# Kernel optimization log

Hardware: AMD Instinct MI355X
Metric: run time of the kernel (lower is better)

## Reference

```python
import jax, jax.numpy as jnp
import numpy as np

EPS_LN = 1e-5
EPS_BN = 1e-5


def ln_channels(x, w, b):
    # LayerNorm2d: normalize over channel dim of NCHW
    mu = x.mean(axis=1, keepdims=True)
    var = x.var(axis=1, keepdims=True)
    return (x - mu) / jnp.sqrt(var + EPS_LN) * w[None, :, None, None] + b[None, :, None, None]


def bn_eval(x, g, b):
    # eval-mode BatchNorm2d with running_mean=0, running_var=1
    return x / jnp.sqrt(1.0 + EPS_BN) * g[None, :, None, None] + b[None, :, None, None]


def conv1x1(x, w, b):
    return jnp.einsum('bchw,oc->bohw', x, w) + b[None, :, None, None]


def q_shift(x):
    # directional shift: 4 channel quarters shifted right/left/down/up by 1 px (zero pad)
    C = x.shape[1]
    q = C // 4
    return jnp.concatenate([
        jnp.pad(x[:, 0 * q:1 * q, :, :-1], ((0, 0), (0, 0), (0, 0), (1, 0))),
        jnp.pad(x[:, 1 * q:2 * q, :, 1:], ((0, 0), (0, 0), (0, 0), (0, 1))),
        jnp.pad(x[:, 2 * q:3 * q, :-1, :], ((0, 0), (0, 0), (1, 0), (0, 0))),
        jnp.pad(x[:, 3 * q:4 * q, 1:, :], ((0, 0), (0, 0), (0, 1), (0, 0))),
    ], axis=1)


def wkv_scan(k, v, w_neg, u):
    # numerically-stable RWKV WKV recurrence. k, v: [N, T, C]; w_neg (negative decay), u: [C]
    N, T, C = k.shape

    def step(carry, kv):
        a, b, p = carry
        kt, vt = kv
        q = jnp.maximum(p, u + kt)
        e1 = jnp.exp(p - q)
        e2 = jnp.exp(u + kt - q)
        out = (e1 * a + e2 * vt) / (e1 * b + e2)
        q2 = jnp.maximum(p + w_neg, kt)
        f1 = jnp.exp(p + w_neg - q2)
        f2 = jnp.exp(kt - q2)
        return (f1 * a + f2 * vt, f1 * b + f2, q2), out

    init = (jnp.zeros((N, C), k.dtype), jnp.zeros((N, C), k.dtype), jnp.full((N, C), -1e38, k.dtype))
    _, outs = jax.lax.scan(step, init, (jnp.swapaxes(k, 0, 1), jnp.swapaxes(v, 0, 1)))
    return jnp.swapaxes(outs, 0, 1)


def shape_guided_rwkv(x, mask, mix_k, mix_v, mix_r, Wk, Wv, Wr, Wo, decay, first, kn_w, kn_b):
    B, C, H, W = x.shape
    xs = q_shift(x)
    x_sh = mask * xs + (1.0 - mask) * x  # saliency-guided shift blend
    mk = mix_k[None, :, None, None]
    mv = mix_v[None, :, None, None]
    mr = mix_r[None, :, None, None]
    xk = x * mk + x_sh * (1.0 - mk)
    xv = x * mv + x_sh * (1.0 - mv)
    xr = x * mr + x_sh * (1.0 - mr)
    k = jnp.einsum('bchw,oc->bohw', xk, Wk)
    v = jnp.einsum('bchw,oc->bohw', xv, Wv)
    sr = jax.nn.sigmoid(jnp.einsum('bchw,oc->bohw', xr, Wr))
    w_neg = -jnp.exp(decay)
    # horizontal orientation: scan each row left->right
    kh = k.transpose(0, 2, 3, 1).reshape(B * H, W, C)
    vh = v.transpose(0, 2, 3, 1).reshape(B * H, W, C)
    wkv_h = wkv_scan(kh, vh, w_neg, first).reshape(B, H, W, C).transpose(0, 3, 1, 2)
    # vertical orientation: scan each column top->bottom
    kv_ = k.transpose(0, 3, 2, 1).reshape(B * W, H, C)
    vv_ = v.transpose(0, 3, 2, 1).reshape(B * W, H, C)
    wkv_v = wkv_scan(kv_, vv_, w_neg, first).reshape(B, W, H, C).transpose(0, 3, 2, 1)
    wkv = 0.5 * (wkv_h + wkv_v)
    wkv = ln_channels(wkv, kn_w, kn_b)  # key_norm=True
    out = jnp.einsum('bchw,oc->bohw', sr * wkv, Wo)
    return x + out


def channel_fusion(x, c1_w, c1_b, bn1_g, bn1_b, c2_w, c2_b, bn2_g, bn2_b, c3_w, c3_b, bn3_g, bn3_b):
    # grouped 3x3 conv (groups=2) -> GELU -> BN -> 1x1 expand -> GELU -> BN -> 1x1 reduce -> GELU -> BN
    y = jax.lax.conv_general_dilated(x, c1_w, (1, 1), 'SAME',
                                     dimension_numbers=('NCHW', 'OIHW', 'NCHW'),
                                     feature_group_count=2) + c1_b[None, :, None, None]
    y = bn_eval(jax.nn.gelu(y, approximate=False), bn1_g, bn1_b)
    y = bn_eval(jax.nn.gelu(conv1x1(y, c2_w, c2_b), approximate=False), bn2_g, bn2_b)
    y = bn_eval(jax.nn.gelu(conv1x1(y, c3_w, c3_b), approximate=False), bn3_g, bn3_b)
    return y


def patch_expand(x, up_w, up_b, s=2):
    B, C, H, W = x.shape
    y = conv1x1(x, up_w, up_b)  # [B, Cout*s*s, H, W]
    Cout = y.shape[1] // (s * s)
    y = y.reshape(B, Cout, s, s, H, W).transpose(0, 1, 4, 2, 5, 3).reshape(B, Cout, H * s, W * s)
    return y


def setup_inputs() -> dict:
    key = jax.random.key(0)
    B, C, Cs, Cout, H, W, s = 8, 256, 512, 128, 64, 64, 2
    ks = jax.random.split(key, 32)
    sc = C ** -0.5
    inp = {
        'x': jax.random.normal(ks[0], (B, C, H, W), jnp.float32),
        'skip': jax.random.normal(ks[1], (B, Cs, H, W), jnp.float32),
        'saliency_mask': jax.random.uniform(ks[2], (B, 1, H, W), jnp.float32),
        'ln1_w': jnp.ones((C,)), 'ln1_b': jnp.zeros((C,)),
        'ln2_w': jnp.ones((C,)), 'ln2_b': jnp.zeros((C,)),
        'mix_k': jax.random.uniform(ks[3], (C,)),
        'mix_v': jax.random.uniform(ks[4], (C,)),
        'mix_r': jax.random.uniform(ks[5], (C,)),
        'Wk': jax.random.normal(ks[6], (C, C)) * sc,
        'Wv': jax.random.normal(ks[7], (C, C)) * sc,
        'Wr': jax.random.normal(ks[8], (C, C)) * sc,
        'Wo': jax.random.normal(ks[9], (C, C)) * sc,
        'decay': jax.random.normal(ks[10], (C,)) * 0.5,
        'first': jax.random.normal(ks[11], (C,)) * 0.5,
        'kn_w': jnp.ones((C,)), 'kn_b': jnp.zeros((C,)),
        'sp_w': jax.random.normal(ks[12], (C, Cs)) * (Cs ** -0.5),
        'sp_b': jnp.zeros((C,)),
        'c1_w': jax.random.normal(ks[13], (2 * C, C, 3, 3)) * ((C * 9) ** -0.5),
        'c1_b': jnp.zeros((2 * C,)),
        'bn1_g': jnp.ones((2 * C,)), 'bn1_b': jnp.zeros((2 * C,)),
        'c2_w': jax.random.normal(ks[14], (4 * C, 2 * C)) * ((2 * C) ** -0.5),
        'c2_b': jnp.zeros((4 * C,)),
        'bn2_g': jnp.ones((4 * C,)), 'bn2_b': jnp.zeros((4 * C,)),
        'c3_w': jax.random.normal(ks[15], (C, 4 * C)) * ((4 * C) ** -0.5),
        'c3_b': jnp.zeros((C,)),
        'bn3_g': jnp.ones((C,)), 'bn3_b': jnp.zeros((C,)),
        'up_w': jax.random.normal(ks[16], (Cout * s * s, C)) * sc,
        'up_b': jnp.zeros((Cout * s * s,)),
    }
    return inp


def reference(x, skip, saliency_mask, ln1_w, ln1_b, ln2_w, ln2_b, mix_k, mix_v, mix_r,
              Wk, Wv, Wr, Wo, decay, first, kn_w, kn_b, sp_w, sp_b,
              c1_w, c1_b, bn1_g, bn1_b, c2_w, c2_b, bn2_g, bn2_b, c3_w, c3_b, bn3_g, bn3_b,
              up_w, up_b):
    xn = ln_channels(x, ln1_w, ln1_b)
    x_sg = shape_guided_rwkv(xn, saliency_mask, mix_k, mix_v, mix_r, Wk, Wv, Wr, Wo,
                             decay, first, kn_w, kn_b)
    skip_feat = conv1x1(skip, sp_w, sp_b)
    x_cat = jnp.concatenate([x_sg, skip_feat], axis=1)
    x_fused = channel_fusion(x_cat, c1_w, c1_b, bn1_g, bn1_b, c2_w, c2_b, bn2_g, bn2_b,
                             c3_w, c3_b, bn3_g, bn3_b)
    x_fused = ln_channels(x_fused, ln2_w, ln2_b)
    return patch_expand(x_fused, up_w, up_b, s=2)
```

## Files before the change

### kernel.cpp

```cpp
#include <hip/hip_runtime.h>
#include <hip/hip_bf16.h>
#include <math.h>

#define B_ 8
#define C_ 256
#define P_ 4096

typedef __bf16 bf16_t;
typedef __attribute__((ext_vector_type(8))) __bf16 bf16x8;
typedef __attribute__((ext_vector_type(4))) __bf16 bf16x4;
typedef __attribute__((ext_vector_type(4))) float f32x4;

template<typename T, int TRANS, int TROUT>
__global__ __launch_bounds__(256)
void ln_stats_kernel(const T* __restrict__ in, float2* __restrict__ stats,
                     bf16_t* __restrict__ outT)
{
    __shared__ float sred[4][64];
    __shared__ float s2red[4][64];
    int tid = threadIdx.x;
    if (TRANS) {
        int wp = tid >> 2, cw = tid & 3;
        int gp = blockIdx.x * 64 + wp;
        const bf16_t* row = (const bf16_t*)in + (size_t)gp * 256 + cw * 64;
        float s = 0.f, s2 = 0.f;
        #pragma unroll
        for (int i = 0; i < 64; i += 8) {
            bf16x8 v = *reinterpret_cast<const bf16x8*>(&row[i]);
            #pragma unroll
            for (int j = 0; j < 8; ++j) {
                float f = (float)v[j]; s += f; s2 += f * f;
            }
        }
        sred[cw][wp] = s; s2red[cw][wp] = s2;
        __syncthreads();
        if (cw == 0) {
            s  = sred[0][wp]  + sred[1][wp]  + sred[2][wp]  + sred[3][wp];
            s2 = s2red[0][wp] + s2red[1][wp] + s2red[2][wp] + s2red[3][wp];
            float mu  = s * (1.f / 256.f);
            float var = s2 * (1.f / 256.f) - mu * mu;
            stats[gp] = make_float2(mu, 1.0f / sqrtf(var + 1e-5f));
        }
        return;
    }
    int wp = tid & 63, cw = tid >> 6;
    int gp = blockIdx.x * 64 + wp;
    int b  = gp >> 12, p = gp & 4095;
    size_t base = (size_t)b * 256 * 4096 + p;
    float s = 0.f, s2 = 0.f;
    bf16x8 chunk;
    #pragma unroll 8
    for (int cc = 0; cc < 64; ++cc) {
        float v = (float)in[base + (size_t)(cw * 64 + cc) * 4096];
        s += v; s2 += v * v;
        if (TROUT) {
            chunk[cc & 7] = (bf16_t)v;
            if ((cc & 7) == 7)
                *reinterpret_cast<bf16x8*>(
                    &outT[(size_t)gp * 256 + cw * 64 + (cc & ~7)]) = chunk;
        }
    }
    sred[cw][wp] = s; s2red[cw][wp] = s2;
    __syncthreads();
    if (cw == 0) {
        s  = sred[0][wp]  + sred[1][wp]  + sred[2][wp]  + sred[3][wp];
        s2 = s2red[0][wp] + s2red[1][wp] + s2red[2][wp] + s2red[3][wp];
        float mu  = s * (1.f / 256.f);
        float var = s2 * (1.f / 256.f) - mu * mu;
        stats[gp] = make_float2(mu, 1.0f / sqrtf(var + 1e-5f));
    }
}

__global__ __launch_bounds__(256)
void skip_transpose_kernel(const float* __restrict__ in, bf16_t* __restrict__ outT)
{
    __shared__ bf16_t t[64 * 66];
    int p0 = blockIdx.x << 6;
    int c0 = blockIdx.y << 6;
    int b  = blockIdx.z;
    int tid = threadIdx.x;
    int pl = tid & 63, cq = tid >> 6;
    const float* src = in + ((size_t)b * 512 + c0) * 4096 + p0;
    #pragma unroll
    for (int i = 0; i < 16; ++i) {
        int cl = i * 4 + cq;
        t[pl * 66 + cl] = (bf16_t)src[(size_t)cl * 4096 + pl];
    }
    __syncthreads();
    int pw = tid >> 2, ch = tid & 3;
    bf16x8 v0 = *reinterpret_cast<const bf16x8*>(&t[pw * 66 + ch * 16]);
    bf16x8 v1 = *reinterpret_cast<const bf16x8*>(&t[pw * 66 + ch * 16 + 8]);
    bf16_t* dst = outT + ((size_t)b * 4096 + p0 + pw) * 512 + c0 + ch * 16;
    *reinterpret_cast<bf16x8*>(dst) = v0;
    *reinterpret_cast<bf16x8*>(dst + 8) = v1;
}

__global__ __launch_bounds__(256)
void qshift_mix_kernel(const float* __restrict__ x, const float2* __restrict__ st1,
                       const float* __restrict__ mask,
                       const float* __restrict__ gw, const float* __restrict__ gb,
                       const float* __restrict__ mk_, const float* __restrict__ mv_,
                       const float* __restrict__ mr_,
                       bf16_t* __restrict__ xk, bf16_t* __restrict__ xv,
                       bf16_t* __restrict__ xr)
{
    int gid = blockIdx.x * 256 + threadIdx.x;
    int g = gid << 3;
    int p = g & 4095;
    int c = (g >> 12) & 255;
    int b = g >> 20;
    int h = p >> 6, w0 = p & 63;
    float gwc = gw[c], gbc = gb[c];
    int sbase = (b << 12) + p;

    float4 x0 = *reinterpret_cast<const float4*>(&x[g]);
    float4 x1 = *reinterpret_cast<const float4*>(&x[g + 4]);
    float xv8[8] = {x0.x, x0.y, x0.z, x0.w, x1.x, x1.y, x1.z, x1.w};
    float2 s8[8];
    #pragma unroll
    for (int i = 0; i < 4; ++i) {
        float4 t = *reinterpret_cast<const float4*>(&st1[sbase + i * 2]);
        s8[2 * i]     = make_float2(t.x, t.y);
        s8[2 * i + 1] = make_float2(t.z, t.w);
    }
    float xn8[8];
    #pragma unroll
    for (int i = 0; i < 8; ++i)
        xn8[i] = (xv8[i] - s8[i].x) * s8[i].y * gwc + gbc;

    float xs8[8];
    int quad = c >> 6;
    if (quad == 0) {
        xs8[0] = 0.f;
        if (w0 > 0) {
            float xm = x[g - 1]; float2 sm = st1[sbase - 1];
            xs8[0] = (xm - sm.x) * sm.y * gwc + gbc;
        }
        #pragma unroll
        for (int i = 1; i < 8; ++i) xs8[i] = xn8[i - 1];
    } else if (quad == 1) {
        #pragma unroll
        for (int i = 0; i < 7; ++i) xs8[i] = xn8[i + 1];
        xs8[7] = 0.f;
        if (w0 + 8 < 64) {
            float xp = x[g + 8]; float2 sp = st1[sbase + 8];
            xs8[7] = (xp - sp.x) * sp.y * gwc + gbc;
        }
    } else {
        int d = (quad == 2) ? -64 : 64;
        bool ok = (quad == 2) ? (h > 0) : (h < 63);
        if (ok) {
            float4 y0 = *reinterpret_cast<const float4*>(&x[g + d]);
            float4 y1 = *reinterpret_cast<const float4*>(&x[g + d + 4]);
            float yv8[8] = {y0.x, y0.y, y0.z, y0.w, y1.x, y1.y, y1.z, y1.w};
            #pragma unroll
            for (int i = 0; i < 4; ++i) {
                float4 t = *reinterpret_cast<const float4*>(&st1[sbase + d + i * 2]);
                float2 sa = make_float2(t.x, t.y), sb = make_float2(t.z, t.w);
                xs8[2 * i]     = (yv8[2 * i]     - sa.x) * sa.y * gwc + gbc;
                xs8[2 * i + 1] = (yv8[2 * i + 1] - sb.x) * sb.y * gwc + gbc;
            }
        } else {
            #pragma unroll
            for (int i = 0; i < 8; ++i) xs8[i] = 0.f;
        }
    }

    float4 m0 = *reinterpret_cast<const float4*>(&mask[sbase]);
    float4 m1 = *reinterpret_cast<const float4*>(&mask[sbase + 4]);
    float mm[8] = {m0.x, m0.y, m0.z, m0.w, m1.x, m1.y, m1.z, m1.w};
    float xsh8[8];
    #pragma unroll
    for (int i = 0; i < 8; ++i)
        xsh8[i] = mm[i] * xs8[i] + (1.f - mm[i]) * xn8[i];

    float ak = mk_[c], av = mv_[c], ar = mr_[c];
    bf16x8 ok_, ov_, or_;
    #pragma unroll
    for (int i = 0; i < 8; ++i) {
        ok_[i] = (bf16_t)(ak * xn8[i] + (1.f - ak) * xsh8[i]);
        ov_[i] = (bf16_t)(av * xn8[i] + (1.f - av) * xsh8[i]);
        or_[i] = (bf16_t)(ar * xn8[i] + (1.f - ar) * xsh8[i]);
    }
    *reinterpret_cast<bf16x8*>(&xk[g]) = ok_;
    *reinterpret_cast<bf16x8*>(&xv[g]) = ov_;
    *reinterpret_cast<bf16x8*>(&xr[g]) = or_;
}

#define EP_NONE    0
#define EP_SIGMOID 1
#define EP_BIAS    2
#define EP_RESLN   3
#define EP_GELU_BN 4
#define EP_SHUFFLE 5
#define EP_KVR     6
#define EP_WOSKIP  7

template<int NB, int BMODE, int EPI, int OUTBF, int TILE, int OTR>
__global__ __launch_bounds__(256, (TILE == 64) ? 4 : 2)
void mfma_gemm(const bf16_t* __restrict__ Wp, const void* __restrict__ Xin,
               const bf16_t* __restrict__ X2,
               const float2* __restrict__ bstats, const float* __restrict__ blnw,
               const float* __restrict__ blnb,
               const float* __restrict__ bias, const bf16_t* __restrict__ skipT,
               const float* __restrict__ bng, const float* __restrict__ bnb,
               const float* __restrict__ resx, const float2* __restrict__ estats,
               const float* __restrict__ elnw, const float* __restrict__ elnb,
               void* __restrict__ OutV,
               int O, int K, int Cstride, int obs, int ocoff)
{
    constexpr int MI = TILE / 32;
    constexpr int BROWS = (NB == 3) ? 2 * 66 : TILE;
    __shared__ bf16_t Alds[NB * TILE * 36];
    __shared__ bf16_t Blds[BROWS * 36];
    int tid = threadIdx.x;
    int bx = blockIdx.x;
    int o0 = blockIdx.y * TILE;
    int b  = blockIdx.z;
    int p0 = bx * TILE;
    int cbase = (NB == 3) ? ((o0 >> 8) << 8) : 0;

    bool wo = true;
    int bb = b;
    if (EPI == EP_WOSKIP) { wo = (b >> 3) != 0; bb = b & 7; }

    const bf16_t* Wpe = Wp;
    if (EPI == EP_KVR)    Wpe = Wp + (size_t)(b >> 3) * O * K;
    if (EPI == EP_WOSKIP) Wpe = wo ? Wp : (Wp + 65536);
    int Krun = K;
    if (EPI == EP_WOSKIP) Krun = wo ? 256 : 512;

    int lane = tid & 63, wid = tid >> 6;
    int l15 = lane & 15;
    int lk8 = (lane >> 4) << 3;
    int mbase = (wid >> 1) * (TILE / 2);
    int nbase = (wid & 1) * (TILE / 2);

    const bf16_t* Xb_bf = (const bf16_t*)Xin + (size_t)bb * Cstride * 4096;
    const float*  Xb_f  = (const float*)Xin + (size_t)bb * Cstride * 4096;
    const bf16_t* X2b   = (BMODE == 3) ? X2 + (size_t)bb * Cstride * 4096 : nullptr;
    const bf16_t* skb   = (EPI == EP_WOSKIP)
                          ? skipT + (size_t)bb * 4096 * 512 : nullptr;

    f32x4 acc[MI][MI] = {};

    if (NB == 3 && tid < 144) {
        int r = tid / 72, rest = tid % 72;
        int col = rest / 36, cc = rest % 36;
        Blds[(r * 66 + (col ? 65 : 0)) * 36 + cc] = (bf16_t)0.f;
    }

    for (int kh = 0; kh < NB; ++kh) {
        for (int c0 = 0; c0 < Krun; c0 += 32) {
            __syncthreads();
            if (NB == 3) {
                #pragma unroll
                for (int q = 0; q < 2; ++q) {
                    int cid = tid + q * 256;
                    int r   = cid >> 8;
                    int w   = (cid >> 2) & 63;
                    int ch4 = cid & 3;
                    int hr  = (bx << 1) + kh - 1 + r;
                    bf16x8 bv;
                    #pragma unroll
                    for (int i = 0; i < 8; ++i) bv[i] = (bf16_t)0.f;
                    if (hr >= 0 && hr < 64)
                        bv = *reinterpret_cast<const bf16x8*>(
                               Xb_bf + (size_t)((hr << 6) + w) * 512
                                     + cbase + c0 + ch4 * 8);
                    *reinterpret_cast<bf16x8*>(
                        &Blds[(r * 66 + w + 1) * 36 + ch4 * 8]) = bv;
                }
            } else if (BMODE >= 4) {
                constexpr int NCH = (TILE == 128) ? 2 : 1;
                #pragma unroll
                for (int q = 0; q < NCH; ++q) {
                    int cid = tid + q * 256;
                    int p   = cid >> 2;
                    int ch4 = cid & 3;
                    bf16x8 bv = *reinterpret_cast<const bf16x8*>(
                        Xb_bf + (size_t)(p0 + p) * Cstride + c0 + ch4 * 8);
                    if (BMODE == 5) {
                        float2 st = bstats[(bb << 12) + p0 + p];
                        #pragma unroll
                        for (int j = 0; j < 8; ++j) {
                            int cc = c0 + ch4 * 8 + j;
                            bv[j] = (bf16_t)(((float)bv[j] - st.x) * st.y
                                             * blnw[cc] + blnb[cc]);
                        }
                    }
                    *reinterpret_cast<bf16x8*>(&Blds[p * 36 + ch4 * 8]) = bv;
                }
            } else if (EPI == EP_WOSKIP) {
                int p = tid >> 2, ch4 = tid & 3;
                if (!wo) {
                    bf16x8 bv = *reinterpret_cast<const bf16x8*>(
                        skb + (size_t)(p0 + p) * 512 + c0 + ch4 * 8);
                    *reinterpret_cast<bf16x8*>(&Blds[p * 36 + ch4 * 8]) = bv;
                } else {
                    bf16x8 wv = *reinterpret_cast<const bf16x8*>(
                        Xb_bf + (size_t)(p0 + p) * 256 + c0 + ch4 * 8);
                    bf16x8 rv = *reinterpret_cast<const bf16x8*>(
                        X2b + (size_t)(p0 + p) * 256 + c0 + ch4 * 8);
                    float2 st = bstats[(bb << 12) + p0 + p];
                    bf16x8 bv;
                    #pragma unroll
                    for (int j = 0; j < 8; ++j) {
                        int cc = c0 + ch4 * 8 + j;
                        float v = ((float)wv[j] - st.x) * st.y * blnw[cc] + blnb[cc];
                        v *= (float)rv[j];
                        bv[j] = (bf16_t)v;
                    }
                    *reinterpret_cast<bf16x8*>(&Blds[p * 36 + ch4 * 8]) = bv;
                }
            } else {
                int p_loc = tid & (TILE - 1);
                #pragma unroll
                for (int rep = 0; rep < (TILE == 128 ? 2 : 1); ++rep) {
                    int cgr = (TILE == 128) ? ((tid >> 7) + rep * 2) : (tid >> 6);
                    bf16x8 bv;
                    size_t gbase = (size_t)(c0 + cgr * 8) * 4096 + p0 + p_loc;
                    #pragma unroll
                    for (int j = 0; j < 8; ++j) {
                        size_t gi = gbase + (size_t)j * 4096;
                        if (BMODE == 0) bv[j] = Xb_bf[gi];
                        else            bv[j] = (bf16_t)Xb_f[gi];
                    }
                    *reinterpret_cast<bf16x8*>(&Blds[p_loc * 36 + cgr * 8]) = bv;
                }
            }
            if (TILE == 128) {
                int ao = tid >> 1, aq = tid & 1;
                #pragma unroll
                for (int t = 0; t < NB; ++t) {
                    const bf16_t* wsrc = (NB == 3)
                        ? Wpe + ((size_t)(kh * 3 + t) * O + o0 + ao) * 256 + c0
                        : Wpe + (size_t)(o0 + ao) * Krun + c0;
                    bf16x8 w0 = *reinterpret_cast<const bf16x8*>(wsrc + aq * 8);
                    bf16x8 w1 = *reinterpret_cast<const bf16x8*>(wsrc + (aq + 2) * 8);
                    *reinterpret_cast<bf16x8*>(&Alds[(t * 128 + ao) * 36 + aq * 8]) = w0;
                    *reinterpret_cast<bf16x8*>(&Alds[(t * 128 + ao) * 36 + (aq + 2) * 8]) = w1;
                }
            } else {
                int ao = tid >> 2, aq = tid & 3;
                const bf16_t* wsrc = Wpe + (size_t)(o0 + ao) * Krun + c0;
                bf16x8 w0 = *reinterpret_cast<const bf16x8*>(wsrc + aq * 8);
                *reinterpret_cast<bf16x8*>(&Alds[ao * 36 + aq * 8]) = w0;
            }
            __syncthreads();
            #pragma unroll
            for (int t = 0; t < NB; ++t) {
                bf16x8 af[MI];
                #pragma unroll
                for (int i = 0; i < MI; ++i)
                    af[i] = *reinterpret_cast<const bf16x8*>(
                              &Alds[(t * TILE + mbase + i * 16 + l15) * 36 + lk8]);
                #pragma unroll
                for (int j = 0; j < MI; ++j) {
                    int pl = nbase + j * 16;
                    int baddr;
                    if (NB == 3)
                        baddr = ((pl >> 6) * 66 + (pl & 63) + l15 + t) * 36 + lk8;
                    else
                        baddr = (pl + l15) * 36 + lk8;
                    bf16x8 bfv = *reinterpret_cast<const bf16x8*>(&Blds[baddr]);
                    #pragma unroll
                    for (int i = 0; i < MI; ++i)
                        acc[i][j] = __builtin_amdgcn_mfma_f32_16x16x32_bf16(
                                        af[i], bfv, acc[i][j], 0, 0, 0);
                }
            }
        }
    }

    const float bnsc = 1.0f / sqrtf(1.f + 1e-5f);

    if (EPI == EP_KVR && b >= 16) {
        bf16_t* rT = (bf16_t*)OutV + (size_t)16 * 256 * 4096;
        #pragma unroll
        for (int i = 0; i < MI; ++i) {
            int ob = o0 + mbase + i * 16 + ((lane >> 4) << 2);
            #pragma unroll
            for (int j = 0; j < MI; ++j) {
                int pp = p0 + nbase + j * 16 + l15;
                bf16x4 pk;
                #pragma unroll
                for (int r = 0; r < 4; ++r) {
                    float t = acc[i][j][r];
                    pk[r] = (bf16_t)(1.f / (1.f + expf(-t)));
                }
                *reinterpret_cast<bf16x4*>(
                    &rT[((size_t)(b - 16) * 4096 + pp) * 256 + ob]) = pk;
            }
        }
        return;
    }

    if (EPI == EP_WOSKIP) {
        int oco = wo ? 0 : 256;
        #pragma unroll
        for (int i = 0; i < MI; ++i) {
            int ob = o0 + mbase + i * 16 + ((lane >> 4) << 2);
            float bi4[4], rw4[4], rb4[4];
            #pragma unroll
            for (int r = 0; r < 4; ++r) {
                bi4[r] = wo ? 0.f : bias[ob + r];
                rw4[r] = wo ? elnw[ob + r] : 0.f;
                rb4[r] = wo ? elnb[ob + r] : 0.f;
            }
            #pragma unroll
            for (int j = 0; j < MI; ++j) {
                int pp = p0 + nbase + j * 16 + l15;
                float2 st = make_float2(0.f, 1.f);
                if (wo) st = estats[(bb << 12) + pp];
                bf16x4 pk;
                #pragma unroll
                for (int r = 0; r < 4; ++r) {
                    float t = acc[i][j][r];
                    if (!wo) {
                        t += bi4[r];
                    } else {
                        float rv = resx[((size_t)bb * 256 + ob + r) * 4096 + pp];
                        t += (rv - st.x) * st.y * rw4[r] + rb4[r];
                    }
                    pk[r] = (bf16_t)t;
                }
                *reinterpret_cast<bf16x4*>(
                    &((bf16_t*)OutV)[((size_t)bb * 4096 + pp) * 512 + oco + ob]) = pk;
            }
        }
        return;
    }

    if (EPI == EP_GELU_BN && OTR) {
        #pragma unroll
        for (int i = 0; i < MI; ++i) {
            int ob = o0 + mbase + i * 16 + ((lane >> 4) << 2);
            float bi4[4], sc4[4], sh4[4];
            #pragma unroll
            for (int r = 0; r < 4; ++r) {
                bi4[r] = bias[ob + r];
                sc4[r] = bng[ob + r] * bnsc;
                sh4[r] = bnb[ob + r];
            }
            #pragma unroll
            for (int j = 0; j < MI; ++j) {
                int pp = p0 + nbase + j * 16 + l15;
                bf16x4 pk;
                #pragma unroll
                for (int r = 0; r < 4; ++r) {
                    float t = acc[i][j][r] + bi4[r];
                    t = 0.5f * t * (1.f + erff(t * 0.70710678118654752f));
                    pk[r] = (bf16_t)(t * sc4[r] + sh4[r]);
                }
                *reinterpret_cast<bf16x4*>(
                    &((bf16_t*)OutV)[((size_t)bb * 4096 + pp) * obs + ocoff + ob]) = pk;
            }
        }
        return;
    }

    #pragma unroll
    for (int i = 0; i < MI; ++i) {
        #pragma unroll
        for (int r = 0; r < 4; ++r) {
            int o = o0 + mbase + i * 16 + ((lane >> 4) << 2) + r;
            float bi = 0.f;
            if (EPI == EP_BIAS || EPI == EP_GELU_BN || EPI == EP_SHUFFLE) bi = bias[o];
            float sc = 0.f, sh = 0.f;
            if (EPI == EP_GELU_BN) { sc = bng[o] * bnsc; sh = bnb[o]; }
            #pragma unroll
            for (int j = 0; j < MI; ++j) {
                int pp = p0 + nbase + j * 16 + l15;
                float t = acc[i][j][r];
                if (EPI == EP_SIGMOID) t = 1.f / (1.f + expf(-t));
                if (EPI == EP_BIAS || EPI == EP_GELU_BN || EPI == EP_SHUFFLE) t += bi;
                if (EPI == EP_GELU_BN) {
                    t = 0.5f * t * (1.f + erff(t * 0.70710678118654752f));
                    t = t * sc + sh;
                }
                if (EPI == EP_SHUFFLE) {
                    int co = o >> 2, s1 = (o >> 1) & 1, s2 = o & 1;
                    int hh = pp >> 6, ww = pp & 63;
                    ((float*)OutV)[(((size_t)bb * 128 + co) * 128 + hh * 2 + s1) * 128
                                   + ww * 2 + s2] = t;
                } else {
                    size_t oidx = ((size_t)bb * obs + ocoff + o) * 4096 + pp;
                    if (OUTBF) ((bf16_t*)OutV)[oidx] = (bf16_t)t;
                    else       ((float*)OutV)[oidx]  = t;
                }
            }
        }
    }
}

__global__ __launch_bounds__(256)
void pack_all_kernel(const float* __restrict__ wk, const float* __restrict__ wv,
                     const float* __restrict__ wr, const float* __restrict__ wo,
                     const float* __restrict__ sp, const float* __restrict__ c2,
                     const float* __restrict__ c3, const float* __restrict__ up,
                     const float* __restrict__ c1, bf16_t* __restrict__ outfl,
                     bf16_t* __restrict__ outc1)
{
    int g = blockIdx.x * 256 + threadIdx.x;
    if (g < 1310720) {
        float v;
        if      (g < 65536)   v = wk[g];
        else if (g < 131072)  v = wv[g - 65536];
        else if (g < 196608)  v = wr[g - 131072];
        else if (g < 262144)  v = wo[g - 196608];
        else if (g < 393216)  v = sp[g - 262144];
        else if (g < 917504)  v = c2[g - 393216];
        else if (g < 1179648) v = c3[g - 917504];
        else                  v = up[g - 1179648];
        outfl[g] = (bf16_t)v;
    } else {
        int g2 = g - 1310720;
        if (g2 < 1179648) {
            int c = g2 & 255;
            int o = (g2 >> 8) & 511;
            int tap = g2 >> 17;
            outc1[g2] = (bf16_t)c1[(size_t)o * 2304 + c * 9 + tap];
        }
    }
}

__global__ __launch_bounds__(64)
void wkv_merged_kernel(const bf16_t* __restrict__ kin, const bf16_t* __restrict__ vin,
                       bf16_t* __restrict__ outw,
                       const float* __restrict__ decay, const float* __restrict__ first)
{
    __shared__ bf16_t ks[64 * 66];
    __shared__ bf16_t vs[64 * 66];
    __shared__ bf16_t os[64 * 66];
    int c = blockIdx.x;
    int b = blockIdx.y;
    int tid = threadIdx.x;
    size_t base = ((size_t)b * 256 + c) * 4096;

    uint32_t* ksu = (uint32_t*)ks;
    uint32_t* vsu = (uint32_t*)vs;
    uint32_t* osu = (uint32_t*)os;
    #pragma unroll
    for (int i = 0; i < 8; ++i) {
        int idx = i * 512 + tid * 8;
        int row = idx >> 6, col = idx & 63;
        bf16x8 kv = *reinterpret_cast<const bf16x8*>(&kin[base + idx]);
        bf16x8 vv = *reinterpret_cast<const bf16x8*>(&vin[base + idx]);
        uint32_t* kp = (uint32_t*)&kv;
        uint32_t* vp = (uint32_t*)&vv;
        #pragma unroll
        for (int q = 0; q < 4; ++q) {
            ksu[row * 33 + (col >> 1) + q] = kp[q];
            vsu[row * 33 + (col >> 1) + q] = vp[q];
        }
    }
    __syncthreads();

    float u  = first[c];
    float wn = -expf(decay[c]);

    {
        int h = tid;
        float a = 0.f, bb2 = 0.f, pp = -1e38f;
        for (int w = 0; w < 64; ++w) {
            float kt = (float)ks[h * 66 + w], vt = (float)vs[h * 66 + w];
            float q  = fmaxf(pp, u + kt);
            float e1 = expf(pp - q), e2 = expf(u + kt - q);
            float ov = (e1 * a + e2 * vt) / (e1 * bb2 + e2);
            os[h * 66 + w] = (bf16_t)ov;
            float q2 = fmaxf(pp + wn, kt);
            float f1 = expf(pp + wn - q2), f2 = expf(kt - q2);
            a = f1 * a + f2 * vt;
            bb2 = f1 * bb2 + f2;
            pp = q2;
        }
    }
    __syncthreads();

    {
        int w = tid;
        float a = 0.f, bb2 = 0.f, pp = -1e38f;
        for (int h = 0; h < 64; ++h) {
            float kt = (float)ks[h * 66 + w], vt = (float)vs[h * 66 + w];
            float q  = fmaxf(pp, u + kt);
            float e1 = expf(pp - q), e2 = expf(u + kt - q);
            float ov = (e1 * a + e2 * vt) / (e1 * bb2 + e2);
            os[h * 66 + w] = (bf16_t)(0.5f * ((float)os[h * 66 + w] + ov));
            float q2 = fmaxf(pp + wn, kt);
            float f1 = expf(pp + wn - q2), f2 = expf(kt - q2);
            a = f1 * a + f2 * vt;
            bb2 = f1 * bb2 + f2;
            pp = q2;
        }
    }
    __syncthreads();

    #pragma unroll
    for (int i = 0; i < 8; ++i) {
        int idx = i * 512 + tid * 8;
        int row = idx >> 6, col = idx & 63;
        bf16x8 ov;
        uint32_t* op = (uint32_t*)&ov;
        #pragma unroll
        for (int q = 0; q < 4; ++q)
            op[q] = osu[row * 33 + (col >> 1) + q];
        *reinterpret_cast<bf16x8*>(&outw[base + idx]) = ov;
    }
}

extern "C" void kernel_launch(void* const* d_in, const int* in_sizes, int n_in,
                              void* d_out, int out_size, void* d_ws, size_t ws_size,
                              hipStream_t stream)
{
    const float* x      = (const float*)d_in[0];
    const float* skip   = (const float*)d_in[1];
    const float* mask   = (const float*)d_in[2];
    const float* ln1_w  = (const float*)d_in[3];
    const float* ln1_b  = (const float*)d_in[4];
    const float* ln2_w  = (const float*)d_in[5];
    const float* ln2_b  = (const float*)d_in[6];
    const float* mix_k  = (const float*)d_in[7];
    const float* mix_v  = (const float*)d_in[8];
    const float* mix_r  = (const float*)d_in[9];
    const float* Wk     = (const float*)d_in[10];
    const float* Wv     = (const float*)d_in[11];
    const float* Wr     = (const float*)d_in[12];
    const float* Wo     = (const float*)d_in[13];
    const float* decay  = (const float*)d_in[14];
    const float* first  = (const float*)d_in[15];
    const float* kn_w   = (const float*)d_in[16];
    const float* kn_b   = (const float*)d_in[17];
    const float* sp_w   = (const float*)d_in[18];
    const float* sp_b   = (const float*)d_in[19];
    const float* c1_w   = (const float*)d_in[20];
    const float* c1_b   = (const float*)d_in[21];
    const float* bn1_g  = (const float*)d_in[22];
    const float* bn1_b  = (const float*)d_in[23];
    const float* c2_w   = (const float*)d_in[24];
    const float* c2_b   = (const float*)d_in[25];
    const float* bn2_g  = (const float*)d_in[26];
    const float* bn2_b  = (const float*)d_in[27];
    const float* c3_w   = (const float*)d_in[28];
    const float* c3_b   = (const float*)d_in[29];
    const float* bn3_g  = (const float*)d_in[30];
    const float* bn3_b  = (const float*)d_in[31];
    const float* up_w   = (const float*)d_in[32];
    const float* up_b   = (const float*)d_in[33];
    float* out = (float*)d_out;

    float* ws = (float*)d_ws;
    const size_t S = 8388608;
    const size_t Hs = S / 2;
    bf16_t* xk   = (bf16_t*)ws;
    bf16_t* xv   = (bf16_t*)(ws + Hs);
    bf16_t* xr   = (bf16_t*)(ws + 2 * Hs);
    bf16_t* wkvT = (bf16_t*)(ws + 2 * Hs);
    bf16_t* kbuf = (bf16_t*)(ws + 3 * Hs);
    bf16_t* vbuf = (bf16_t*)(ws + 4 * Hs);
    bf16_t* rbuf = (bf16_t*)(ws + 5 * Hs);
    bf16_t* wkv  = (bf16_t*)(ws + 6 * Hs);
    bf16_t* xcat = (bf16_t*)(ws + 7 * Hs);
    bf16_t* skbf = (bf16_t*)(ws + 9 * Hs);
    bf16_t* y1   = (bf16_t*)(ws + 9 * Hs);
    bf16_t* y2   = (bf16_t*)ws;
    bf16_t* y3   = (bf16_t*)(ws + 4 * Hs);
    float*  wtop = ws + 11 * Hs;
    bf16_t* w9   = (bf16_t*)wtop;
    bf16_t* wfl  = w9 + 1179648;
    float2* st1  = (float2*)(wfl + 1310720);
    float2* stk  = st1 + 32768;
    float2* st2  = stk + 32768;
    bf16_t* wkb = wfl;
    bf16_t* wob = wfl + 196608;
    bf16_t* c2b = wfl + 393216;
    bf16_t* c3b = wfl + 917504;
    bf16_t* upb = wfl + 1179648;

    dim3 blk(256);

    pack_all_kernel<<<dim3(9728), blk, 0, stream>>>(Wk, Wv, Wr, Wo, sp_w, c2_w,
                                                    c3_w, up_w, c1_w, wfl, w9);
    ln_stats_kernel<float, 0, 0><<<dim3(512), blk, 0, stream>>>(x, st1, nullptr);
    skip_transpose_kernel<<<dim3(64, 8, 8), blk, 0, stream>>>(skip, skbf);

    qshift_mix_kernel<<<dim3(4096), blk, 0, stream>>>(x, st1, mask, ln1_w, ln1_b,
                                                      mix_k, mix_v, mix_r, xk, xv, xr);
    mfma_gemm<1, 0, EP_KVR, 1, 64, 0><<<dim3(64, 4, 24), blk, 0, stream>>>(
        wkb, xk, nullptr, nullptr, nullptr, nullptr, nullptr, nullptr, nullptr,
        nullptr, nullptr, nullptr, nullptr, nullptr, kbuf, 256, 256, 256, 256, 0);
    wkv_merged_kernel<<<dim3(256, 8), dim3(64), 0, stream>>>(kbuf, vbuf, wkv, decay, first);
    ln_stats_kernel<bf16_t, 0, 1><<<dim3(512), blk, 0, stream>>>(wkv, stk, wkvT);
    mfma_gemm<1, 3, EP_WOSKIP, 1, 64, 0><<<dim3(64, 4, 16), blk, 0, stream>>>(
        wob, wkvT, rbuf, stk, kn_w, kn_b, sp_b, skbf, nullptr, nullptr,
        x, st1, ln1_w, ln1_b, xcat, 256, 0, 256, 512, 0);
    mfma_gemm<3, 0, EP_GELU_BN, 1, 128, 1><<<dim3(32, 4, 8), blk, 0, stream>>>(
        w9, xcat, nullptr, nullptr, nullptr, nullptr, c1_b, nullptr, bn1_g, bn1_b,
        nullptr, nullptr, nullptr, nullptr, y1, 512, 256, 512, 512, 0);
    mfma_gemm<1, 4, EP_GELU_BN, 1, 128, 1><<<dim3(32, 8, 8), blk, 0, stream>>>(
        c2b, y1, nullptr, nullptr, nullptr, nullptr, c2_b, nullptr, bn2_g, bn2_b,
        nullptr, nullptr, nullptr, nullptr, y2, 1024, 512, 512, 1024, 0);
    mfma_gemm<1, 4, EP_GELU_BN, 1, 64, 1><<<dim3(64, 4, 8), blk, 0, stream>>>(
        c3b, y2, nullptr, nullptr, nullptr, nullptr, c3_b, nullptr, bn3_g, bn3_b,
        nullptr, nullptr, nullptr, nullptr, y3, 256, 1024, 1024, 256, 0);
    ln_stats_kernel<bf16_t, 1, 0><<<dim3(512), blk, 0, stream>>>(y3, st2, nullptr);
    mfma_gemm<1, 5, EP_SHUFFLE, 0, 64, 0><<<dim3(64, 8, 8), blk, 0, stream>>>(
        upb, y3, nullptr, st2, ln2_w, ln2_b, up_b, nullptr, nullptr, nullptr,
        nullptr, nullptr, nullptr, nullptr, out, 512, 256, 256, 0, 0);
}
```

Before: 474.5 us.

## Add dedicated 3x3 grouped conv kernel loading 4 input rows once per K-chunk

Replaces the generic mfma_gemm NB=3 path for the 3x3 conv with a dedicated conv9_kernel. It stages all 4 needed input rows and all 9 tap weight tiles once per 32-channel chunk, then runs all 9 taps from LDS, instead of reloading 2 rows per kh pass. The output tile changes from 128x128 to 64 outputs by 128 pixels, which doubles the grid in the channel dimension. The generic GEMM loses its NB==3 code, which simplifies it. The larger LDS footprint (about 58KB) may limit occupancy.

```diff
diff --git a/kernel.cpp b/kernel.cpp
--- a/kernel.cpp
+++ b/kernel.cpp
@@ -187,6 +187,110 @@
     *reinterpret_cast<bf16x8*>(&xr[g]) = or_;
 }
 
+__global__ __launch_bounds__(256, 2)
+void conv9_kernel(const bf16_t* __restrict__ Wp, const bf16_t* __restrict__ XinT,
+                  const float* __restrict__ bias, const float* __restrict__ bng,
+                  const float* __restrict__ bnb, bf16_t* __restrict__ OutT)
+{
+    __shared__ bf16_t Alds[9 * 64 * 36];
+    __shared__ bf16_t Blds[4 * 66 * 36];
+    int tid = threadIdx.x;
+    int bx = blockIdx.x;
+    int o0 = blockIdx.y * 64;
+    int b  = blockIdx.z;
+    int p0 = bx << 7;
+    int cbase = (o0 >> 8) << 8;
+
+    int lane = tid & 63, wid = tid >> 6;
+    int l15 = lane & 15;
+    int lk8 = (lane >> 4) << 3;
+    int mbase = (wid >> 1) << 5;
+    int nbase = (wid & 1) << 6;
+
+    const bf16_t* Xb = XinT + (size_t)b * 4096 * 512;
+
+    f32x4 acc[2][4] = {};
+
+    for (int f = tid; f < 288; f += 256) {
+        int rr = f / 72, rest = f % 72;
+        int col = rest / 36, cc = rest % 36;
+        Blds[(rr * 66 + (col ? 65 : 0)) * 36 + cc] = (bf16_t)0.f;
+    }
+
+    int wpos = tid >> 2, ch4 = tid & 3;
+    int ao = tid >> 2, aq = tid & 3;
+
+    for (int c0 = 0; c0 < 256; c0 += 32) {
+        __syncthreads();
+        #pragma unroll
+        for (int rr = 0; rr < 4; ++rr) {
+            int hr = (bx << 1) + rr - 1;
+            bf16x8 bv;
+            #pragma unroll
+            for (int i = 0; i < 8; ++i) bv[i] = (bf16_t)0.f;
+            if (hr >= 0 && hr < 64)
+                bv = *reinterpret_cast<const bf16x8*>(
+                       Xb + (size_t)((hr << 6) + wpos) * 512 + cbase + c0 + ch4 * 8);
+            *reinterpret_cast<bf16x8*>(&Blds[(rr * 66 + wpos + 1) * 36 + ch4 * 8]) = bv;
+        }
+        #pragma unroll
+        for (int t = 0; t < 9; ++t) {
+            bf16x8 wv = *reinterpret_cast<const bf16x8*>(
+                Wp + ((size_t)t * 512 + o0 + ao) * 256 + c0 + aq * 8);
+            *reinterpret_cast<bf16x8*>(&Alds[(t * 64 + ao) * 36 + aq * 8]) = wv;
+        }
+        __syncthreads();
+        #pragma unroll
+        for (int kh = 0; kh < 3; ++kh) {
+            #pragma unroll
+            for (int kw = 0; kw < 3; ++kw) {
+                int t = kh * 3 + kw;
+                bf16x8 af[2];
+                #pragma unroll
+                for (int i = 0; i < 2; ++i)
+                    af[i] = *reinterpret_cast<const bf16x8*>(
+                              &Alds[(t * 64 + mbase + i * 16 + l15) * 36 + lk8]);
+                #pragma unroll
+                for (int j = 0; j < 4; ++j) {
+                    int pl = nbase + j * 16;
+                    int baddr = (((pl >> 6) + kh) * 66 + (pl & 63) + l15 + kw) * 36 + lk8;
+                    bf16x8 bfv = *reinterpret_cast<const bf16x8*>(&Blds[baddr]);
+                    #pragma unroll
+                    for (int i = 0; i < 2; ++i)
+                        acc[i][j] = __builtin_amdgcn_mfma_f32_16x16x32_bf16(
+                                        af[i], bfv, acc[i][j], 0, 0, 0);
+                }
+            }
+        }
+    }
+
+    const float bnsc = 1.0f / sqrtf(1.f + 1e-5f);
+    #pragma unroll
+    for (int i = 0; i < 2; ++i) {
+        int ob = o0 + mbase + i * 16 + ((lane >> 4) << 2);
+        float bi4[4], sc4[4], sh4[4];
+        #pragma unroll
+        for (int r = 0; r < 4; ++r) {
+            bi4[r] = bias[ob + r];
+            sc4[r] = bng[ob + r] * bnsc;
+            sh4[r] = bnb[ob + r];
+        }
+        #pragma unroll
+        for (int j = 0; j < 4; ++j) {
+            int pp = p0 + nbase + j * 16 + l15;
+            bf16x4 pk;
+            #pragma unroll
+            for (int r = 0; r < 4; ++r) {
+                float t = acc[i][j][r] + bi4[r];
+                t = 0.5f * t * (1.f + erff(t * 0.70710678118654752f));
+                pk[r] = (bf16_t)(t * sc4[r] + sh4[r]);
+            }
+            *reinterpret_cast<bf16x4*>(
+                &OutT[((size_t)b * 4096 + pp) * 512 + ob]) = pk;
+        }
+    }
+}
+
 #define EP_NONE    0
 #define EP_SIGMOID 1
 #define EP_BIAS    2
@@ -210,7 +314,7 @@
                int O, int K, int Cstride, int obs, int ocoff)
 {
     constexpr int MI = TILE / 32;
-    constexpr int BROWS = (NB == 3) ? 2 * 66 : TILE;
+    constexpr int BROWS = TILE;
     __shared__ bf16_t Alds[NB * TILE * 36];
     __shared__ bf16_t Blds[BROWS * 36];
     int tid = threadIdx.x;
@@ -218,7 +322,6 @@
     int o0 = blockIdx.y * TILE;
     int b  = blockIdx.z;
     int p0 = bx * TILE;
-    int cbase = (NB == 3) ? ((o0 >> 8) << 8) : 0;
 
     bool wo = true;
     int bb = b;
@@ -244,132 +347,94 @@
 
     f32x4 acc[MI][MI] = {};
 
-    if (NB == 3 && tid < 144) {
-        int r = tid / 72, rest = tid % 72;
-        int col = rest / 36, cc = rest % 36;
-        Blds[(r * 66 + (col ? 65 : 0)) * 36 + cc] = (bf16_t)0.f;
-    }
-
-    for (int kh = 0; kh < NB; ++kh) {
-        for (int c0 = 0; c0 < Krun; c0 += 32) {
-            __syncthreads();
-            if (NB == 3) {
-                #pragma unroll
-                for (int q = 0; q < 2; ++q) {
-                    int cid = tid + q * 256;
-                    int r   = cid >> 8;
-                    int w   = (cid >> 2) & 63;
-                    int ch4 = cid & 3;
-                    int hr  = (bx << 1) + kh - 1 + r;
-                    bf16x8 bv;
-                    #pragma unroll
-                    for (int i = 0; i < 8; ++i) bv[i] = (bf16_t)0.f;
-                    if (hr >= 0 && hr < 64)
-                        bv = *reinterpret_cast<const bf16x8*>(
-                               Xb_bf + (size_t)((hr << 6) + w) * 512
-                                     + cbase + c0 + ch4 * 8);
-                    *reinterpret_cast<bf16x8*>(
-                        &Blds[(r * 66 + w + 1) * 36 + ch4 * 8]) = bv;
-                }
-            } else if (BMODE >= 4) {
-                constexpr int NCH = (TILE == 128) ? 2 : 1;
-                #pragma unroll
-                for (int q = 0; q < NCH; ++q) {
-                    int cid = tid + q * 256;
-                    int p   = cid >> 2;
-                    int ch4 = cid & 3;
-                    bf16x8 bv = *reinterpret_cast<const bf16x8*>(
-                        Xb_bf + (size_t)(p0 + p) * Cstride + c0 + ch4 * 8);
-                    if (BMODE == 5) {
-                        float2 st = bstats[(bb << 12) + p0 + p];
-                        #pragma unroll
-                        for (int j = 0; j < 8; ++j) {
-                            int cc = c0 + ch4 * 8 + j;
-                            bv[j] = (bf16_t)(((float)bv[j] - st.x) * st.y
-                                             * blnw[cc] + blnb[cc]);
-                        }
-                    }
-                    *reinterpret_cast<bf16x8*>(&Blds[p * 36 + ch4 * 8]) = bv;
-                }
-            } else if (EPI == EP_WOSKIP) {
-                int p = tid >> 2, ch4 = tid & 3;
-                if (!wo) {
-                    bf16x8 bv = *reinterpret_cast<const bf16x8*>(
-                        skb + (size_t)(p0 + p) * 512 + c0 + ch4 * 8);
-                    *reinterpret_cast<bf16x8*>(&Blds[p * 36 + ch4 * 8]) = bv;
-                } else {
-                    bf16x8 wv = *reinterpret_cast<const bf16x8*>(
-                        Xb_bf + (size_t)(p0 + p) * 256 + c0 + ch4 * 8);
-                    bf16x8 rv = *reinterpret_cast<const bf16x8*>(
-                        X2b + (size_t)(p0 + p) * 256 + c0 + ch4 * 8);
+    for (int c0 = 0; c0 < Krun; c0 += 32) {
+        __syncthreads();
+        if (BMODE >= 4) {
+            constexpr int NCH = (TILE == 128) ? 2 : 1;
+            #pragma unroll
+            for (int q = 0; q < NCH; ++q) {
+                int cid = tid + q * 256;
+                int p   = cid >> 2;
+                int ch4 = cid & 3;
+                bf16x8 bv = *reinterpret_cast<const bf16x8*>(
+                    Xb_bf + (size_t)(p0 + p) * Cstride + c0 + ch4 * 8);
+                if (BMODE == 5) {
                     float2 st = bstats[(bb << 12) + p0 + p];
-                    bf16x8 bv;
                     #pragma unroll
                     for (int j = 0; j < 8; ++j) {
                         int cc = c0 + ch4 * 8 + j;
-                        float v = ((float)wv[j] - st.x) * st.y * blnw[cc] + blnb[cc];
-                        v *= (float)rv[j];
-                        bv[j] = (bf16_t)v;
+                        bv[j] = (bf16_t)(((float)bv[j] - st.x) * st.y
+                                         * blnw[cc] + blnb[cc]);
                     }
-                    *reinterpret_cast<bf16x8*>(&Blds[p * 36 + ch4 * 8]) = bv;
-                }
+                }
+                *reinterpret_cast<bf16x8*>(&Blds[p * 36 + ch4 * 8]) = bv;
+            }
+        } else if (EPI == EP_WOSKIP) {
+            int p = tid >> 2, ch4 = tid & 3;
+            if (!wo) {
+                bf16x8 bv = *reinterpret_cast<const bf16x8*>(
+                    skb + (size_t)(p0 + p) * 512 + c0 + ch4 * 8);
+                *reinterpret_cast<bf16x8*>(&Blds[p * 36 + ch4 * 8]) = bv;
             } else {
-                int p_loc = tid & (TILE - 1);
+                bf16x8 wv = *reinterpret_cast<const bf16x8*>(
+                    Xb_bf + (size_t)(p0 + p) * 256 + c0 + ch4 * 8);
+                bf16x8 rv = *reinterpret_cast<const bf16x8*>(
+                    X2b + (size_t)(p0 + p) * 256 + c0 + ch4 * 8);
+                float2 st = bstats[(bb << 12) + p0 + p];
+                bf16x8 bv;
                 #pragma unroll
-                for (int rep = 0; rep < (TILE == 128 ? 2 : 1); ++rep) {
-                    int cgr = (TILE == 128) ? ((tid >> 7) + rep * 2) : (tid >> 6);
-                    bf16x8 bv;
-                    size_t gbase = (size_t)(c0 + cgr * 8) * 4096 + p0 + p_loc;
-                    #pragma unroll
-                    for (int j = 0; j < 8; ++j) {
-                        size_t gi = gbase + (size_t)j * 4096;
-                        if (BMODE == 0) bv[j] = Xb_bf[gi];
-                        else            bv[j] = (bf16_t)Xb_f[gi];
-                    }
-                    *reinterpret_cast<bf16x8*>(&Blds[p_loc * 36 + cgr * 8]) = bv;
-                }
-            }
-            if (TILE == 128) {
-                int ao = tid >> 1, aq = tid & 1;
+                for (int j = 0; j < 8; ++j) {
+                    int cc = c0 + ch4 * 8 + j;
+                    float v = ((float)wv[j] - st.x) * st.y * blnw[cc] + blnb[cc];
+                    v *= (float)rv[j];
+                    bv[j] = (bf16_t)v;
+                }
+                *reinterpret_cast<bf16x8*>(&Blds[p * 36 + ch4 * 8]) = bv;
+            }
+        } else {
+            int p_loc = tid & (TILE - 1);
+            #pragma unroll
+            for (int rep = 0; rep < (TILE == 128 ? 2 : 1); ++rep) {
+                int cgr = (TILE == 128) ? ((tid >> 7) + rep * 2) : (tid >> 6);
+                bf16x8 bv;
+                size_t gbase = (size_t)(c0 + cgr * 8) * 4096 + p0 + p_loc;
                 #pragma unroll
-                for (int t = 0; t < NB; ++t) {
-                    const bf16_t* wsrc = (NB == 3)
-                        ? Wpe + ((size_t)(kh * 3 + t) * O + o0 + ao) * 256 + c0
-                        : Wpe + (size_t)(o0 + ao) * Krun + c0;
-                    bf16x8 w0 = *reinterpret_cast<const bf16x8*>(wsrc + aq * 8);
-                    bf16x8 w1 = *reinterpret_cast<const bf16x8*>(wsrc + (aq + 2) * 8);
-                    *reinterpret_cast<bf16x8*>(&Alds[(t * 128 + ao) * 36 + aq * 8]) = w0;
-                    *reinterpret_cast<bf16x8*>(&Alds[(t * 128 + ao) * 36 + (aq + 2) * 8]) = w1;
-                }
-            } else {
-                int ao = tid >> 2, aq = tid & 3;
-                const bf16_t* wsrc = Wpe + (size_t)(o0 + ao) * Krun + c0;
-                bf16x8 w0 = *reinterpret_cast<const bf16x8*>(wsrc + aq * 8);
-                *reinterpret_cast<bf16x8*>(&Alds[ao * 36 + aq * 8]) = w0;
-            }
-            __syncthreads();
-            #pragma unroll
-            for (int t = 0; t < NB; ++t) {
-                bf16x8 af[MI];
-                #pragma unroll
-                for (int i = 0; i < MI; ++i)
-                    af[i] = *reinterpret_cast<const bf16x8*>(
-                              &Alds[(t * TILE + mbase + i * 16 + l15) * 36 + lk8]);
-                #pragma unroll
-                for (int j = 0; j < MI; ++j) {
-                    int pl = nbase + j * 16;
-                    int baddr;
-                    if (NB == 3)
-                        baddr = ((pl >> 6) * 66 + (pl & 63) + l15 + t) * 36 + lk8;
-                    else
-                        baddr = (pl + l15) * 36 + lk8;
-                    bf16x8 bfv = *reinterpret_cast<const bf16x8*>(&Blds[baddr]);
-                    #pragma unroll
-                    for (int i = 0; i < MI; ++i)
-                        acc[i][j] = __builtin_amdgcn_mfma_f32_16x16x32_bf16(
-                                        af[i], bfv, acc[i][j], 0, 0, 0);
-                }
-            }
+                for (int j = 0; j < 8; ++j) {
+                    size_t gi = gbase + (size_t)j * 4096;
+                    if (BMODE == 0) bv[j] = Xb_bf[gi];
+                    else            bv[j] = (bf16_t)Xb_f[gi];
+                }
+                *reinterpret_cast<bf16x8*>(&Blds[p_loc * 36 + cgr * 8]) = bv;
+            }
+        }
+        if (TILE == 128) {
+            int ao = tid >> 1, aq = tid & 1;
+            const bf16_t* wsrc = Wpe + (size_t)(o0 + ao) * Krun + c0;
+            bf16x8 w0 = *reinterpret_cast<const bf16x8*>(wsrc + aq * 8);
+            bf16x8 w1 = *reinterpret_cast<const bf16x8*>(wsrc + (aq + 2) * 8);
+            *reinterpret_cast<bf16x8*>(&Alds[ao * 36 + aq * 8]) = w0;
+            *reinterpret_cast<bf16x8*>(&Alds[ao * 36 + (aq + 2) * 8]) = w1;
+        } else {
+            int ao = tid >> 2, aq = tid & 3;
+            const bf16_t* wsrc = Wpe + (size_t)(o0 + ao) * Krun + c0;
+            bf16x8 w0 = *reinterpret_cast<const bf16x8*>(wsrc + aq * 8);
+            *reinterpret_cast<bf16x8*>(&Alds[ao * 36 + aq * 8]) = w0;
+        }
+        __syncthreads();
+        bf16x8 af[MI];
+        #pragma unroll
+        for (int i = 0; i < MI; ++i)
+            af[i] = *reinterpret_cast<const bf16x8*>(
+                      &Alds[(mbase + i * 16 + l15) * 36 + lk8]);
+        #pragma unroll
+        for (int j = 0; j < MI; ++j) {
+            int pl = nbase + j * 16;
+            bf16x8 bfv = *reinterpret_cast<const bf16x8*>(
+                &Blds[(pl + l15) * 36 + lk8]);
+            #pragma unroll
+            for (int i = 0; i < MI; ++i)
+                acc[i][j] = __builtin_amdgcn_mfma_f32_16x16x32_bf16(
+                                af[i], bfv, acc[i][j], 0, 0, 0);
         }
     }
 
@@ -694,9 +759,7 @@
     mfma_gemm<1, 3, EP_WOSKIP, 1, 64, 0><<<dim3(64, 4, 16), blk, 0, stream>>>(
         wob, wkvT, rbuf, stk, kn_w, kn_b, sp_b, skbf, nullptr, nullptr,
         x, st1, ln1_w, ln1_b, xcat, 256, 0, 256, 512, 0);
-    mfma_gemm<3, 0, EP_GELU_BN, 1, 128, 1><<<dim3(32, 4, 8), blk, 0, stream>>>(
-        w9, xcat, nullptr, nullptr, nullptr, nullptr, c1_b, nullptr, bn1_g, bn1_b,
-        nullptr, nullptr, nullptr, nullptr, y1, 512, 256, 512, 512, 0);
+    conv9_kernel<<<dim3(32, 8, 8), blk, 0, stream>>>(w9, xcat, c1_b, bn1_g, bn1_b, y1);
     mfma_gemm<1, 4, EP_GELU_BN, 1, 128, 1><<<dim3(32, 8, 8), blk, 0, stream>>>(
         c2b, y1, nullptr, nullptr, nullptr, nullptr, c2_b, nullptr, bn2_g, bn2_b,
         nullptr, nullptr, nullptr, nullptr, y2, 1024, 512, 512, 1024, 0);
```

Measured after the change: 496.0 us (median of 2 runs). 4.5% more time.
